# Kernel tuning notes

Hardware: AMD Instinct MI355X
Metric: run time of the kernel (lower is better)

The kernel has to match this reference:

```python
import jax, jax.numpy as jnp
import numpy as np

S, X, G = 2048, 2048, 2
INPUT_SIZE = (3, 32, 32)
F = int(np.prod(INPUT_SIZE))


def setup_inputs() -> dict:
    key = jax.random.key(0)
    k1, k2, k3 = jax.random.split(key, 3)
    samples = jax.random.normal(k1, (S,) + INPUT_SIZE, dtype=jnp.float32)
    x = jax.random.normal(k2, (X,) + INPUT_SIZE, dtype=jnp.float32)
    # per-feature std per gradation, kept in [0.1, 1.0) like ranges_std scaling
    std = jax.random.uniform(k3, (G, F), dtype=jnp.float32, minval=0.1, maxval=1.0)
    return {"samples": samples, "x": x, "std": std}


def reference(samples, x, std):
    # samples: [S, C, H, W], x: [X, C, H, W], std: [G, F]
    G_, F_ = std.shape
    s = samples.reshape(samples.shape[0], F_)  # [S, F]
    xf = x.reshape(x.shape[0], F_)             # [X, F]
    w = 1.0 / (std * std)                       # [G, F] precision
    # per-gradation normalizer: -0.5*F*log(2pi) - sum_f log(std)
    const = -0.5 * F_ * jnp.log(2.0 * jnp.pi) - jnp.sum(jnp.log(std), axis=1)  # [G]
    # sum_f -0.5*((s-x)/std)^2 expanded: -0.5*(s^2 w - 2 s w x + x^2 w)
    A = jnp.einsum('sf,gf->gs', s * s, w)        # [G, S]
    C = jnp.einsum('xf,gf->gx', xf * xf, w)      # [G, X]
    B = jnp.einsum('sf,gf,xf->gsx', s, w, xf)    # [G, S, X] cross term
    logits = -0.5 * (A[:, :, None] - 2.0 * B + C[:, None, :]) + const[:, None, None]
    lp = jax.nn.logsumexp(logits, axis=2)        # over x (mixture components)
    lp = jax.nn.logsumexp(lp, axis=0)            # over gradations
    return lp - jnp.log(jnp.float32(x.shape[0] * G_))
```

## Files before the change

kernel.cpp:

```cpp
#include <hip/hip_runtime.h>
#include <math.h>
#include <stdint.h>

#define S_N 2048
#define X_N 2048
#define G_N 2
#define F_N 3072

#define TM 256
#define TN 128
#define BK 64
#define ITERS (F_N / BK)
#define NBUF 3

typedef __bf16 bf16;
typedef __bf16 bf16x4 __attribute__((ext_vector_type(4)));
typedef __bf16 bf16x8 __attribute__((ext_vector_type(8)));
typedef float f32x4 __attribute__((ext_vector_type(4)));
typedef int i32x4 __attribute__((ext_vector_type(4)));

__device__ __forceinline__ void gload_lds16(const bf16* g, void* l) {
  __builtin_amdgcn_global_load_lds(
      (const __attribute__((address_space(1))) void*)g,
      (__attribute__((address_space(3))) void*)l, 16, 0, 0);
}

__global__ void k_const(const float* __restrict__ stdv, float* __restrict__ constg,
                        float* __restrict__ rinv) {
  int g = blockIdx.x;
  int t = threadIdx.x;
  float s = 0.f;
  for (int f = t; f < F_N; f += 256) {
    float v = stdv[g * F_N + f];
    rinv[g * F_N + f] = 1.0f / v;
    s += logf(v);
  }
  for (int o = 32; o; o >>= 1) s += __shfl_xor(s, o);
  __shared__ float red[4];
  int w = t >> 6, l = t & 63;
  if (l == 0) red[w] = s;
  __syncthreads();
  if (t == 0) {
    float tot = red[0] + red[1] + red[2] + red[3];
    constg[g] = -0.5f * (float)F_N * 1.8378770664093453f - tot;
  }
}

__global__ void k_prep(const float* __restrict__ samples, const float* __restrict__ xin,
                       const float* __restrict__ rinv,
                       bf16* __restrict__ U, bf16* __restrict__ V,
                       float* __restrict__ A, float* __restrict__ C) {
  int r = blockIdx.x;
  int t = threadIdx.x;
  bool isS = (r < S_N);
  const float* src = isS ? (samples + (size_t)r * F_N) : (xin + (size_t)(r - S_N) * F_N);
  float4 row[3];
#pragma unroll
  for (int j = 0; j < 3; ++j) row[j] = ((const float4*)src)[t + j * 256];

  __shared__ float red[4];
  int w = t >> 6, l = t & 63;

  for (int g = 0; g < G_N; ++g) {
    const float4* sd = (const float4*)(rinv + (size_t)g * F_N);
    bf16* dst = isS ? (U + ((size_t)g * S_N + r) * F_N)
                    : (V + ((size_t)g * X_N + (r - S_N)) * F_N);
    float acc = 0.f;
#pragma unroll
    for (int j = 0; j < 3; ++j) {
      float4 d = sd[t + j * 256];
      float u0 = row[j].x * d.x;
      float u1 = row[j].y * d.y;
      float u2 = row[j].z * d.z;
      float u3 = row[j].w * d.w;
      bf16x4 b;
      b[0] = (bf16)u0; b[1] = (bf16)u1; b[2] = (bf16)u2; b[3] = (bf16)u3;
      float f0 = (float)b[0], f1 = (float)b[1], f2 = (float)b[2], f3 = (float)b[3];
      acc += f0 * f0 + f1 * f1 + f2 * f2 + f3 * f3;
      ((bf16x4*)dst)[t + j * 256] = b;
    }
    for (int o = 32; o; o >>= 1) acc += __shfl_xor(acc, o);
    __syncthreads();
    if (l == 0) red[w] = acc;
    __syncthreads();
    if (t == 0) {
      float tot = red[0] + red[1] + red[2] + red[3];
      if (isS) A[(size_t)g * S_N + r] = tot;
      else     C[(size_t)g * X_N + (r - S_N)] = tot;
    }
  }
}

__global__ __launch_bounds__(512, 2) void k_gemm(const bf16* __restrict__ U, const bf16* __restrict__ V,
                                                 const float* __restrict__ A, const float* __restrict__ C,
                                                 float* __restrict__ logits) {
  __shared__ i32x4 lds[NBUF * 2048 + NBUF * 1024];
  i32x4* ldsA = lds;
  i32x4* ldsB = lds + NBUF * 2048;

  int t = threadIdx.x;
  int g = blockIdx.z;
  int bm = blockIdx.y * TM;
  int bn = blockIdx.x * TN;

  const bf16* Ub = U + ((size_t)g * S_N + bm) * F_N;
  const bf16* Vb = V + ((size_t)g * X_N + bn) * F_N;

  int wave = t >> 6, lane = t & 63;
  int pos = wave >> 1;
  int kh = wave & 1;
  int wm = pos >> 1;
  int wn = pos & 1;
  int r = lane & 15, q = lane >> 4;
  int fr = (r >> 1) & 7;
  int ck = (kh * 4 + q) ^ fr;
  int abase = (wm * 128 + r) * 8;
  int bbase = (wn * 64 + r) * 8;

  int row0 = t >> 3;
  int gcc = (t & 7) ^ ((t >> 4) & 7);
  const bf16* gA[4];
  const bf16* gB[2];
#pragma unroll
  for (int j = 0; j < 4; ++j) gA[j] = Ub + (size_t)(row0 + j * 64) * F_N + gcc * 8;
#pragma unroll
  for (int j = 0; j < 2; ++j) gB[j] = Vb + (size_t)(row0 + j * 64) * F_N + gcc * 8;

  f32x4 acc[8][4] = {};
  bf16x8 afc[4], afn[4], bE[4], bO[4];

#pragma unroll
  for (int j = 0; j < 4; ++j) gload_lds16(gA[j], &ldsA[0 * 2048 + t + j * 512]);
#pragma unroll
  for (int j = 0; j < 2; ++j) gload_lds16(gB[j], &ldsB[0 * 1024 + t + j * 512]);
#pragma unroll
  for (int j = 0; j < 4; ++j) gload_lds16(gA[j] + BK, &ldsA[1 * 2048 + t + j * 512]);
#pragma unroll
  for (int j = 0; j < 2; ++j) gload_lds16(gB[j] + BK, &ldsB[1 * 1024 + t + j * 512]);
  asm volatile("s_waitcnt vmcnt(6)" ::: "memory");
  __builtin_amdgcn_s_barrier();
#pragma unroll
  for (int mi = 0; mi < 4; ++mi)
    afc[mi] = __builtin_bit_cast(bf16x8, ldsA[abase + mi * 128 + ck]);
#pragma unroll
  for (int ni = 0; ni < 4; ++ni)
    bE[ni] = __builtin_bit_cast(bf16x8, ldsB[bbase + ni * 128 + ck]);

  int cur = 0;

#define KTILE(IT, B_CUR, B_NXT)                                                  \
  {                                                                              \
    int k2 = (IT) + 2;                                                           \
    int pk = (k2 < ITERS ? k2 : 0) * BK;     \
    int stg = (cur >= 1) ? cur - 1 : 2;                           \
    int nxt = (cur == 2) ? 0 : cur + 1;                                          \
    const i32x4* LA  = ldsA + cur * 2048;                                        \
    const i32x4* LAn = ldsA + nxt * 2048;                                        \
    const i32x4* LBn = ldsB + nxt * 1024;                                        \
         \
    gload_lds16(gA[0] + pk, &ldsA[stg * 2048 + t]);                              \
    gload_lds16(gA[1] + pk, &ldsA[stg * 2048 + t + 512]);                        \
    gload_lds16(gA[2] + pk, &ldsA[stg * 2048 + t + 1024]);                       \
    __builtin_amdgcn_s_barrier();                                                \
    _Pragma("unroll")                                                            \
    for (int mi = 0; mi < 4; ++mi)                                               \
      afn[mi] = __builtin_bit_cast(bf16x8, LA[abase + (4 + mi) * 128 + ck]);     \
    __builtin_amdgcn_s_setprio(1);                                               \
    _Pragma("unroll")                                                            \
    for (int mi = 0; mi < 4; ++mi)                                               \
      _Pragma("unroll")                                                          \
      for (int ni = 0; ni < 4; ++ni)                                             \
        acc[mi][ni] = __builtin_amdgcn_mfma_f32_16x16x32_bf16(afc[mi], B_CUR[ni], acc[mi][ni], 0, 0, 0); \
    __builtin_amdgcn_s_setprio(0);                                               \
    __builtin_amdgcn_s_barrier();                                                \
     \
    gload_lds16(gA[3] + pk, &ldsA[stg * 2048 + t + 1536]);                       \
    gload_lds16(gB[0] + pk, &ldsB[stg * 1024 + t]);                              \
    gload_lds16(gB[1] + pk, &ldsB[stg * 1024 + t + 512]);                        \
     \
    asm volatile("s_waitcnt vmcnt(6)" ::: "memory");                             \
    __builtin_amdgcn_s_barrier();  \
    _Pragma("unroll")                                                            \
    for (int mi = 0; mi < 4; ++mi)                                               \
      afc[mi] = __builtin_bit_cast(bf16x8, LAn[abase + mi * 128 + ck]);          \
    _Pragma("unroll")                                                            \
    for (int ni = 0; ni < 4; ++ni)                                               \
      B_NXT[ni] = __builtin_bit_cast(bf16x8, LBn[bbase + ni * 128 + ck]);        \
    __builtin_amdgcn_s_setprio(1);                                               \
    _Pragma("unroll")                                                            \
    for (int mi = 0; mi < 4; ++mi)                                               \
      _Pragma("unroll")                                                          \
      for (int ni = 0; ni < 4; ++ni)                                             \
        acc[4 + mi][ni] = __builtin_amdgcn_mfma_f32_16x16x32_bf16(afn[mi], B_CUR[ni], acc[4 + mi][ni], 0, 0, 0); \
    __builtin_amdgcn_s_setprio(0);                                               \
    __builtin_amdgcn_s_barrier();                                                \
    cur = nxt;                                                                   \
  }

  for (int it0 = 0; it0 < ITERS; it0 += 2) {
    KTILE(it0,     bE, bO)
    KTILE(it0 + 1, bO, bE)
  }
#undef KTILE

  asm volatile("s_waitcnt vmcnt(0) lgkmcnt(0)" ::: "memory");
  __builtin_amdgcn_s_barrier();

  f32x4* scr = (f32x4*)lds;
  {
    f32x4* mw = scr + wave * 1024;
    if (kh == 0) {
#pragma unroll
      for (int mi = 0; mi < 8; ++mi)
#pragma unroll
        for (int nl = 0; nl < 2; ++nl)
          mw[(mi * 2 + nl) * 64 + lane] = acc[mi][2 + nl];
    } else {
#pragma unroll
      for (int mi = 0; mi < 8; ++mi)
#pragma unroll
        for (int nl = 0; nl < 2; ++nl)
          mw[(mi * 2 + nl) * 64 + lane] = acc[mi][nl];
    }
  }
  __syncthreads();
  {
    const f32x4* pw = scr + (wave ^ 1) * 1024;
    if (kh == 0) {
#pragma unroll
      for (int mi = 0; mi < 8; ++mi)
#pragma unroll
        for (int nl = 0; nl < 2; ++nl)
          acc[mi][nl] += pw[(mi * 2 + nl) * 64 + lane];
    } else {
#pragma unroll
      for (int mi = 0; mi < 8; ++mi)
#pragma unroll
        for (int nl = 0; nl < 2; ++nl)
          acc[mi][2 + nl] += pw[(mi * 2 + nl) * 64 + lane];
    }
  }

  const float* Ap = A + (size_t)g * S_N + bm + wm * 128;
  const float* Cp = C + (size_t)g * X_N + bn + wn * 64 + kh * 32;
  float cv[2];
#pragma unroll
  for (int nl = 0; nl < 2; ++nl) cv[nl] = Cp[nl * 16 + r];
#pragma unroll
  for (int mi = 0; mi < 8; ++mi) {
#pragma unroll
    for (int i = 0; i < 4; ++i) {
      int rowl = mi * 16 + q * 4 + i;
      float av = Ap[rowl];
      float* orow = logits + ((size_t)g * S_N + bm + wm * 128 + rowl) * X_N + bn + wn * 64 + kh * 32;
      if (kh == 0) {
        orow[r]      = acc[mi][0][i] - 0.5f * (av + cv[0]);
        orow[16 + r] = acc[mi][1][i] - 0.5f * (av + cv[1]);
      } else {
        orow[r]      = acc[mi][2][i] - 0.5f * (av + cv[0]);
        orow[16 + r] = acc[mi][3][i] - 0.5f * (av + cv[1]);
      }
    }
  }
}

__global__ void k_lse(const float* __restrict__ logits, const float* __restrict__ constg,
                      float* __restrict__ out) {
  int s = blockIdx.x, t = threadIdx.x;
  float c0 = constg[0], c1 = constg[1];
  const float4* p0 = (const float4*)(logits + (size_t)s * X_N);
  const float4* p1 = (const float4*)(logits + ((size_t)S_N + s) * X_N);
  float4 v[4];
  v[0] = p0[t]; v[1] = p0[t + 256];
  v[2] = p1[t]; v[3] = p1[t + 256];
  v[0].x += c0; v[0].y += c0; v[0].z += c0; v[0].w += c0;
  v[1].x += c0; v[1].y += c0; v[1].z += c0; v[1].w += c0;
  v[2].x += c1; v[2].y += c1; v[2].z += c1; v[2].w += c1;
  v[3].x += c1; v[3].y += c1; v[3].z += c1; v[3].w += c1;

  float m = v[0].x;
#pragma unroll
  for (int j = 0; j < 4; ++j) {
    m = fmaxf(m, v[j].x); m = fmaxf(m, v[j].y);
    m = fmaxf(m, v[j].z); m = fmaxf(m, v[j].w);
  }
  for (int o = 32; o; o >>= 1) m = fmaxf(m, __shfl_xor(m, o));
  __shared__ float redm[4];
  __shared__ float reds[4];
  int w = t >> 6, l = t & 63;
  if (l == 0) redm[w] = m;
  __syncthreads();
  m = fmaxf(fmaxf(redm[0], redm[1]), fmaxf(redm[2], redm[3]));

  float sum = 0.f;
#pragma unroll
  for (int j = 0; j < 4; ++j) {
    sum += expf(v[j].x - m) + expf(v[j].y - m) + expf(v[j].z - m) + expf(v[j].w - m);
  }
  for (int o = 32; o; o >>= 1) sum += __shfl_xor(sum, o);
  if (l == 0) reds[w] = sum;
  __syncthreads();
  if (t == 0) {
    float tot = reds[0] + reds[1] + reds[2] + reds[3];
    out[s] = m + logf(tot) - 8.317766166719343f;
  }
}

extern "C" void kernel_launch(void* const* d_in, const int* in_sizes, int n_in,
                              void* d_out, int out_size, void* d_ws, size_t ws_size,
                              hipStream_t stream) {
  const float* samples = (const float*)d_in[0];
  const float* xin     = (const float*)d_in[1];
  const float* stdv    = (const float*)d_in[2];
  float* out = (float*)d_out;

  char* ws = (char*)d_ws;
  size_t off = 0;
  bf16* U = (bf16*)(ws + off);        off += (size_t)G_N * S_N * F_N * 2;
  bf16* V = (bf16*)(ws + off);        off += (size_t)G_N * X_N * F_N * 2;
  float* logits = (float*)(ws + off); off += (size_t)G_N * S_N * X_N * 4;
  float* A = (float*)(ws + off);      off += (size_t)G_N * S_N * 4;
  float* C = (float*)(ws + off);      off += (size_t)G_N * X_N * 4;
  float* constg = (float*)(ws + off); off += 256;
  float* rinv = (float*)(ws + off);   off += (size_t)G_N * F_N * 4;

  k_const<<<dim3(G_N), dim3(256), 0, stream>>>(stdv, constg, rinv);
  k_prep<<<dim3(S_N + X_N), dim3(256), 0, stream>>>(samples, xin, rinv, U, V, A, C);
  k_gemm<<<dim3(X_N / TN, S_N / TM, G_N), dim3(512), 0, stream>>>(U, V, A, C, logits);
  k_lse<<<dim3(S_N), dim3(256), 0, stream>>>(logits, constg, out);
}
```

Measured before the change: 160.1 us.

## Fuse logsumexp partials into GEMM epilogue, drop full logits buffer

The GEMM epilogue now reduces each 32-column slice of logits to a per-row (max, sum-exp) pair with lane shuffles and writes only these partials. A small final kernel merges the 64 partials per gradation across both gradations. This removes the write and re-read of the 32 MB fp32 logits tensor. In exchange the epilogue gains shuffles and exp work and issues strided partial stores.

```diff
diff --git a/kernel.cpp b/kernel.cpp
--- a/kernel.cpp
+++ b/kernel.cpp
@@ -93,7 +93,8 @@
 
 __global__ __launch_bounds__(512, 2) void k_gemm(const bf16* __restrict__ U, const bf16* __restrict__ V,
                                                  const float* __restrict__ A, const float* __restrict__ C,
-                                                 float* __restrict__ logits) {
+                                                 const float* __restrict__ constg,
+                                                 float2* __restrict__ P) {
   __shared__ i32x4 lds[NBUF * 2048 + NBUF * 1024];
   i32x4* ldsA = lds;
   i32x4* ldsB = lds + NBUF * 2048;
@@ -241,69 +242,48 @@
     }
   }
 
+  float cg = constg[g];
+  int slice = (bn >> 5) + wn * 2 + kh;
   const float* Ap = A + (size_t)g * S_N + bm + wm * 128;
   const float* Cp = C + (size_t)g * X_N + bn + wn * 64 + kh * 32;
+  float2* Pw = P + ((size_t)g * S_N + bm + wm * 128) * 64 + slice;
   float cv[2];
-#pragma unroll
-  for (int nl = 0; nl < 2; ++nl) cv[nl] = Cp[nl * 16 + r];
+  cv[0] = Cp[r]; cv[1] = Cp[16 + r];
 #pragma unroll
   for (int mi = 0; mi < 8; ++mi) {
 #pragma unroll
     for (int i = 0; i < 4; ++i) {
       int rowl = mi * 16 + q * 4 + i;
       float av = Ap[rowl];
-      float* orow = logits + ((size_t)g * S_N + bm + wm * 128 + rowl) * X_N + bn + wn * 64 + kh * 32;
-      if (kh == 0) {
-        orow[r]      = acc[mi][0][i] - 0.5f * (av + cv[0]);
-        orow[16 + r] = acc[mi][1][i] - 0.5f * (av + cv[1]);
-      } else {
-        orow[r]      = acc[mi][2][i] - 0.5f * (av + cv[0]);
-        orow[16 + r] = acc[mi][3][i] - 0.5f * (av + cv[1]);
-      }
-    }
-  }
-}
-
-__global__ void k_lse(const float* __restrict__ logits, const float* __restrict__ constg,
-                      float* __restrict__ out) {
-  int s = blockIdx.x, t = threadIdx.x;
-  float c0 = constg[0], c1 = constg[1];
-  const float4* p0 = (const float4*)(logits + (size_t)s * X_N);
-  const float4* p1 = (const float4*)(logits + ((size_t)S_N + s) * X_N);
-  float4 v[4];
-  v[0] = p0[t]; v[1] = p0[t + 256];
-  v[2] = p1[t]; v[3] = p1[t + 256];
-  v[0].x += c0; v[0].y += c0; v[0].z += c0; v[0].w += c0;
-  v[1].x += c0; v[1].y += c0; v[1].z += c0; v[1].w += c0;
-  v[2].x += c1; v[2].y += c1; v[2].z += c1; v[2].w += c1;
-  v[3].x += c1; v[3].y += c1; v[3].z += c1; v[3].w += c1;
-
-  float m = v[0].x;
-#pragma unroll
-  for (int j = 0; j < 4; ++j) {
-    m = fmaxf(m, v[j].x); m = fmaxf(m, v[j].y);
-    m = fmaxf(m, v[j].z); m = fmaxf(m, v[j].w);
-  }
-  for (int o = 32; o; o >>= 1) m = fmaxf(m, __shfl_xor(m, o));
-  __shared__ float redm[4];
-  __shared__ float reds[4];
-  int w = t >> 6, l = t & 63;
-  if (l == 0) redm[w] = m;
-  __syncthreads();
-  m = fmaxf(fmaxf(redm[0], redm[1]), fmaxf(redm[2], redm[3]));
-
-  float sum = 0.f;
-#pragma unroll
-  for (int j = 0; j < 4; ++j) {
-    sum += expf(v[j].x - m) + expf(v[j].y - m) + expf(v[j].z - m) + expf(v[j].w - m);
-  }
+      float v0, v1;
+      if (kh == 0) { v0 = acc[mi][0][i]; v1 = acc[mi][1][i]; }
+      else         { v0 = acc[mi][2][i]; v1 = acc[mi][3][i]; }
+      v0 -= 0.5f * (av + cv[0]);
+      v1 -= 0.5f * (av + cv[1]);
+      float m2 = fmaxf(v0, v1);
+      m2 = fmaxf(m2, __shfl_xor(m2, 1));
+      m2 = fmaxf(m2, __shfl_xor(m2, 2));
+      m2 = fmaxf(m2, __shfl_xor(m2, 4));
+      m2 = fmaxf(m2, __shfl_xor(m2, 8));
+      float l2 = expf(v0 - m2) + expf(v1 - m2);
+      l2 += __shfl_xor(l2, 1);
+      l2 += __shfl_xor(l2, 2);
+      l2 += __shfl_xor(l2, 4);
+      l2 += __shfl_xor(l2, 8);
+      if (r == 0) Pw[(size_t)rowl * 64] = make_float2(m2 + cg, l2);
+    }
+  }
+}
+
+__global__ void k_fin(const float2* __restrict__ P, float* __restrict__ out) {
+  int s = blockIdx.x, l = threadIdx.x;
+  float2 a = P[((size_t)0 * S_N + s) * 64 + l];
+  float2 b = P[((size_t)1 * S_N + s) * 64 + l];
+  float M = fmaxf(a.x, b.x);
+  for (int o = 32; o; o >>= 1) M = fmaxf(M, __shfl_xor(M, o));
+  float sum = a.y * expf(a.x - M) + b.y * expf(b.x - M);
   for (int o = 32; o; o >>= 1) sum += __shfl_xor(sum, o);
-  if (l == 0) reds[w] = sum;
-  __syncthreads();
-  if (t == 0) {
-    float tot = reds[0] + reds[1] + reds[2] + reds[3];
-    out[s] = m + logf(tot) - 8.317766166719343f;
-  }
+  if (l == 0) out[s] = M + logf(sum) - 8.317766166719343f;
 }
 
 extern "C" void kernel_launch(void* const* d_in, const int* in_sizes, int n_in,
@@ -318,7 +298,7 @@
   size_t off = 0;
   bf16* U = (bf16*)(ws + off);        off += (size_t)G_N * S_N * F_N * 2;
   bf16* V = (bf16*)(ws + off);        off += (size_t)G_N * X_N * F_N * 2;
-  float* logits = (float*)(ws + off); off += (size_t)G_N * S_N * X_N * 4;
+  float2* P = (float2*)(ws + off);    off += (size_t)G_N * S_N * 64 * 8;
   float* A = (float*)(ws + off);      off += (size_t)G_N * S_N * 4;
   float* C = (float*)(ws + off);      off += (size_t)G_N * X_N * 4;
   float* constg = (float*)(ws + off); off += 256;
@@ -326,6 +306,6 @@
 
   k_const<<<dim3(G_N), dim3(256), 0, stream>>>(stdv, constg, rinv);
   k_prep<<<dim3(S_N + X_N), dim3(256), 0, stream>>>(samples, xin, rinv, U, V, A, C);
-  k_gemm<<<dim3(X_N / TN, S_N / TM, G_N), dim3(512), 0, stream>>>(U, V, A, C, logits);
-  k_lse<<<dim3(S_N), dim3(256), 0, stream>>>(logits, constg, out);
-}
+  k_gemm<<<dim3(X_N / TN, S_N / TM, G_N), dim3(512), 0, stream>>>(U, V, A, C, constg, P);
+  k_fin<<<dim3(S_N), dim3(64), 0, stream>>>(P, out);
+}
```

Result: slower. 167.7 us (+4.7%).

## Fuse constant computation into prep kernel and fold normalizer into A

Applied to the files above, without the earlier changes.

Removes the separate k_const launch. Each prep block now recomputes 1/std and the summed log(std) into LDS, and the block layout changes so one block handles 16 rows with 32 lanes per row. Each sample row is read once and produces both gradations' scaled bf16 rows in one pass. The per-gradation normalizer is folded into A, so the logsumexp kernel no longer adds constants per element. The cost is redundant reciprocal and log work on std in all 256 blocks, and a larger LDS footprint per block.

```diff
diff --git a/kernel.cpp b/kernel.cpp
--- a/kernel.cpp
+++ b/kernel.cpp
@@ -25,69 +25,62 @@
       (__attribute__((address_space(3))) void*)l, 16, 0, 0);
 }
 
-__global__ void k_const(const float* __restrict__ stdv, float* __restrict__ constg,
-                        float* __restrict__ rinv) {
-  int g = blockIdx.x;
+__global__ __launch_bounds__(512) void k_prep(
+    const float* __restrict__ samples, const float* __restrict__ xin,
+    const float* __restrict__ stdv,
+    bf16* __restrict__ U, bf16* __restrict__ V,
+    float* __restrict__ A, float* __restrict__ C) {
+  __shared__ float rlds[6432];
   int t = threadIdx.x;
-  float s = 0.f;
-  for (int f = t; f < F_N; f += 256) {
-    float v = stdv[g * F_N + f];
-    rinv[g * F_N + f] = 1.0f / v;
-    s += logf(v);
-  }
-  for (int o = 32; o; o >>= 1) s += __shfl_xor(s, o);
-  __shared__ float red[4];
-  int w = t >> 6, l = t & 63;
-  if (l == 0) red[w] = s;
+  int bid = blockIdx.x;
+  int lane = t & 63, wv = t >> 6;
+
+  for (int i = t; i < 2 * F_N; i += 512) rlds[i] = 1.0f / stdv[i];
+
+  float sl0 = 0.f, sl1 = 0.f;
+  for (int i = t; i < F_N; i += 512) {
+    sl0 += logf(stdv[i]);
+    sl1 += logf(stdv[F_N + i]);
+  }
+  for (int o = 32; o; o >>= 1) { sl0 += __shfl_xor(sl0, o); sl1 += __shfl_xor(sl1, o); }
+  if (lane == 0) { rlds[6400 + wv] = sl0; rlds[6408 + wv] = sl1; }
   __syncthreads();
-  if (t == 0) {
-    float tot = red[0] + red[1] + red[2] + red[3];
-    constg[g] = -0.5f * (float)F_N * 1.8378770664093453f - tot;
-  }
-}
-
-__global__ void k_prep(const float* __restrict__ samples, const float* __restrict__ xin,
-                       const float* __restrict__ rinv,
-                       bf16* __restrict__ U, bf16* __restrict__ V,
-                       float* __restrict__ A, float* __restrict__ C) {
-  int r = blockIdx.x;
-  int t = threadIdx.x;
-  bool isS = (r < S_N);
-  const float* src = isS ? (samples + (size_t)r * F_N) : (xin + (size_t)(r - S_N) * F_N);
-  float4 row[3];
-#pragma unroll
-  for (int j = 0; j < 3; ++j) row[j] = ((const float4*)src)[t + j * 256];
-
-  __shared__ float red[4];
-  int w = t >> 6, l = t & 63;
-
-  for (int g = 0; g < G_N; ++g) {
-    const float4* sd = (const float4*)(rinv + (size_t)g * F_N);
-    bf16* dst = isS ? (U + ((size_t)g * S_N + r) * F_N)
-                    : (V + ((size_t)g * X_N + (r - S_N)) * F_N);
-    float acc = 0.f;
-#pragma unroll
-    for (int j = 0; j < 3; ++j) {
-      float4 d = sd[t + j * 256];
-      float u0 = row[j].x * d.x;
-      float u1 = row[j].y * d.y;
-      float u2 = row[j].z * d.z;
-      float u3 = row[j].w * d.w;
-      bf16x4 b;
-      b[0] = (bf16)u0; b[1] = (bf16)u1; b[2] = (bf16)u2; b[3] = (bf16)u3;
-      float f0 = (float)b[0], f1 = (float)b[1], f2 = (float)b[2], f3 = (float)b[3];
-      acc += f0 * f0 + f1 * f1 + f2 * f2 + f3 * f3;
-      ((bf16x4*)dst)[t + j * 256] = b;
-    }
-    for (int o = 32; o; o >>= 1) acc += __shfl_xor(acc, o);
-    __syncthreads();
-    if (l == 0) red[w] = acc;
-    __syncthreads();
-    if (t == 0) {
-      float tot = red[0] + red[1] + red[2] + red[3];
-      if (isS) A[(size_t)g * S_N + r] = tot;
-      else     C[(size_t)g * X_N + (r - S_N)] = tot;
-    }
+  float t0 = 0.f, t1 = 0.f;
+#pragma unroll
+  for (int w2 = 0; w2 < 8; ++w2) { t0 += rlds[6400 + w2]; t1 += rlds[6408 + w2]; }
+  const float KLOG = -0.5f * (float)F_N * 1.8378770664093453f;
+  float c0 = KLOG - t0, c1 = KLOG - t1;
+
+  int l32 = t & 31;
+  int rr = bid * 16 + (t >> 5);
+  bool isS = rr < S_N;
+  int rx = isS ? rr : rr - S_N;
+  const float* src = isS ? samples + (size_t)rx * F_N : xin + (size_t)rx * F_N;
+  bf16* d0 = isS ? U + (size_t)rx * F_N : V + (size_t)rx * F_N;
+  bf16* d1 = isS ? U + ((size_t)S_N + rx) * F_N : V + ((size_t)X_N + rx) * F_N;
+  float a0 = 0.f, a1 = 0.f;
+#pragma unroll 4
+  for (int k = 0; k < 24; ++k) {
+    int c4 = l32 + k * 32;
+    float4 sv = ((const float4*)src)[c4];
+    float4 q0 = ((const float4*)rlds)[c4];
+    float4 q1 = ((const float4*)rlds)[768 + c4];
+    bf16x4 b0, b1;
+    b0[0] = (bf16)(sv.x * q0.x); b0[1] = (bf16)(sv.y * q0.y);
+    b0[2] = (bf16)(sv.z * q0.z); b0[3] = (bf16)(sv.w * q0.w);
+    b1[0] = (bf16)(sv.x * q1.x); b1[1] = (bf16)(sv.y * q1.y);
+    b1[2] = (bf16)(sv.z * q1.z); b1[3] = (bf16)(sv.w * q1.w);
+    float f0 = (float)b0[0], f1 = (float)b0[1], f2 = (float)b0[2], f3 = (float)b0[3];
+    a0 += f0 * f0 + f1 * f1 + f2 * f2 + f3 * f3;
+    float h0 = (float)b1[0], h1 = (float)b1[1], h2 = (float)b1[2], h3 = (float)b1[3];
+    a1 += h0 * h0 + h1 * h1 + h2 * h2 + h3 * h3;
+    ((bf16x4*)d0)[c4] = b0;
+    ((bf16x4*)d1)[c4] = b1;
+  }
+  for (int o = 16; o; o >>= 1) { a0 += __shfl_xor(a0, o); a1 += __shfl_xor(a1, o); }
+  if (l32 == 0) {
+    if (isS) { A[rx] = a0 - 2.f * c0; A[S_N + rx] = a1 - 2.f * c1; }
+    else     { C[rx] = a0;            C[X_N + rx] = a1; }
   }
 }
 
@@ -244,8 +237,7 @@
   const float* Ap = A + (size_t)g * S_N + bm + wm * 128;
   const float* Cp = C + (size_t)g * X_N + bn + wn * 64 + kh * 32;
   float cv[2];
-#pragma unroll
-  for (int nl = 0; nl < 2; ++nl) cv[nl] = Cp[nl * 16 + r];
+  cv[0] = Cp[r]; cv[1] = Cp[16 + r];
 #pragma unroll
   for (int mi = 0; mi < 8; ++mi) {
 #pragma unroll
@@ -264,19 +256,13 @@
   }
 }
 
-__global__ void k_lse(const float* __restrict__ logits, const float* __restrict__ constg,
-                      float* __restrict__ out) {
+__global__ void k_lse(const float* __restrict__ logits, float* __restrict__ out) {
   int s = blockIdx.x, t = threadIdx.x;
-  float c0 = constg[0], c1 = constg[1];
   const float4* p0 = (const float4*)(logits + (size_t)s * X_N);
   const float4* p1 = (const float4*)(logits + ((size_t)S_N + s) * X_N);
   float4 v[4];
   v[0] = p0[t]; v[1] = p0[t + 256];
   v[2] = p1[t]; v[3] = p1[t + 256];
-  v[0].x += c0; v[0].y += c0; v[0].z += c0; v[0].w += c0;
-  v[1].x += c0; v[1].y += c0; v[1].z += c0; v[1].w += c0;
-  v[2].x += c1; v[2].y += c1; v[2].z += c1; v[2].w += c1;
-  v[3].x += c1; v[3].y += c1; v[3].z += c1; v[3].w += c1;
 
   float m = v[0].x;
 #pragma unroll
@@ -321,11 +307,8 @@
   float* logits = (float*)(ws + off); off += (size_t)G_N * S_N * X_N * 4;
   float* A = (float*)(ws + off);      off += (size_t)G_N * S_N * 4;
   float* C = (float*)(ws + off);      off += (size_t)G_N * X_N * 4;
-  float* constg = (float*)(ws + off); off += 256;
-  float* rinv = (float*)(ws + off);   off += (size_t)G_N * F_N * 4;
-
-  k_const<<<dim3(G_N), dim3(256), 0, stream>>>(stdv, constg, rinv);
-  k_prep<<<dim3(S_N + X_N), dim3(256), 0, stream>>>(samples, xin, rinv, U, V, A, C);
+
+  k_prep<<<dim3(256), dim3(512), 0, stream>>>(samples, xin, stdv, U, V, A, C);
   k_gemm<<<dim3(X_N / TN, S_N / TM, G_N), dim3(512), 0, stream>>>(U, V, A, C, logits);
-  k_lse<<<dim3(S_N), dim3(256), 0, stream>>>(logits, constg, out);
-}
+  k_lse<<<dim3(S_N), dim3(256), 0, stream>>>(logits, out);
+}
```

Result: no change. 158.6 us (-1.0%).
